# Kernel optimization log

Measured on AMD Instinct MI355X. Metric: run time of the kernel, lower is better.

## Reference

```python
import jax, jax.numpy as jnp
import numpy as np

N_PE = 100000   # num 'pe' nodes
N_R = 100000    # num 'router' nodes
E = 600000      # edges per relation
D_IN = 64       # input feature dim per node type
H = 128         # hidden_channels
G = 64          # graphs in batch


def setup_inputs() -> dict:
    key = jax.random.key(0)
    ks = jax.random.split(key, 20)
    inp = {}
    inp["x_pe"] = jax.random.normal(ks[0], (N_PE, D_IN), jnp.float32)
    inp["x_r"] = jax.random.normal(ks[1], (N_R, D_IN), jnp.float32)
    # edge_index per relation: row0 = src node ids, row1 = dst node ids
    inp["ei_per"] = jax.random.randint(ks[2], (2, E), 0, N_PE, jnp.int32)   # pe -> router
    inp["ei_rpe"] = jax.random.randint(ks[3], (2, E), 0, N_R, jnp.int32)    # router -> pe
    inp["ei_rr"] = jax.random.randint(ks[4], (2, E), 0, N_R, jnp.int32)     # router -> router
    inp["batch_pe"] = jnp.sort(jax.random.randint(ks[5], (N_PE,), 0, G, jnp.int32))
    inp["batch_r"] = jnp.sort(jax.random.randint(ks[6], (N_R,), 0, G, jnp.int32))
    # GraphConv params, relation axis ordered [pe->router, router->pe, router->router]
    s1 = 1.0 / np.sqrt(D_IN)
    s2 = 1.0 / np.sqrt(H)
    inp["Wrel1"] = jax.random.normal(ks[7], (3, D_IN, H), jnp.float32) * s1
    inp["brel1"] = jnp.zeros((3, H), jnp.float32)
    inp["Wroot1"] = jax.random.normal(ks[8], (3, D_IN, H), jnp.float32) * s1
    inp["Wrel23"] = jax.random.normal(ks[9], (2, 3, H, H), jnp.float32) * s2
    inp["brel23"] = jnp.zeros((2, 3, H), jnp.float32)
    inp["Wroot23"] = jax.random.normal(ks[10], (2, 3, H, H), jnp.float32) * s2
    # per-node-type MLP heads, type axis ordered [pe, router]
    inp["mlp_W1"] = jax.random.normal(ks[11], (2, H, 5), jnp.float32) * s2
    inp["mlp_b1"] = jnp.zeros((2, 5), jnp.float32)
    inp["mlp_W2"] = jax.random.normal(ks[12], (2, 5, 1), jnp.float32) * (1.0 / np.sqrt(5.0))
    inp["mlp_b2"] = jnp.zeros((2, 1), jnp.float32)
    inp["out_W"] = jax.random.normal(ks[13], (2, 1), jnp.float32) * (1.0 / np.sqrt(2.0))
    inp["out_b"] = jnp.zeros((1,), jnp.float32)
    return inp


def _hetero_graphconv(x_pe, x_r, ei_per, ei_rpe, ei_rr, Wrel, brel, Wroot):
    # GraphConv: lin_rel(scatter_add(x_src)) + lin_root(x_dst); to_hetero sums per dst type.
    agg_r_from_pe = jax.ops.segment_sum(x_pe[ei_per[0]], ei_per[1], num_segments=N_R)
    agg_pe_from_r = jax.ops.segment_sum(x_r[ei_rpe[0]], ei_rpe[1], num_segments=N_PE)
    agg_r_from_r = jax.ops.segment_sum(x_r[ei_rr[0]], ei_rr[1], num_segments=N_R)
    o_pe = agg_pe_from_r @ Wrel[1] + brel[1] + x_pe @ Wroot[1]
    o_r = (agg_r_from_pe @ Wrel[0] + brel[0] + x_r @ Wroot[0]) \
        + (agg_r_from_r @ Wrel[2] + brel[2] + x_r @ Wroot[2])
    return o_pe, o_r


def reference(x_pe, x_r, ei_per, ei_rpe, ei_rr, batch_pe, batch_r,
              Wrel1, brel1, Wroot1, Wrel23, brel23, Wroot23,
              mlp_W1, mlp_b1, mlp_W2, mlp_b2, out_W, out_b):
    h_pe, h_r = _hetero_graphconv(x_pe, x_r, ei_per, ei_rpe, ei_rr, Wrel1, brel1, Wroot1)
    h_pe, h_r = jax.nn.relu(h_pe), jax.nn.relu(h_r)
    h_pe, h_r = _hetero_graphconv(h_pe, h_r, ei_per, ei_rpe, ei_rr, Wrel23[0], brel23[0], Wroot23[0])
    h_pe, h_r = jax.nn.relu(h_pe), jax.nn.relu(h_r)
    h_pe, h_r = _hetero_graphconv(h_pe, h_r, ei_per, ei_rpe, ei_rr, Wrel23[1], brel23[1], Wroot23[1])
    gm_pe = jax.ops.segment_max(h_pe, batch_pe, num_segments=G)  # [G, H]
    gm_r = jax.ops.segment_max(h_r, batch_r, num_segments=G)
    def mlp(x, W1, b1, W2, b2):
        return jax.nn.relu(x @ W1 + b1) @ W2 + b2
    o_pe = mlp(gm_pe, mlp_W1[0], mlp_b1[0], mlp_W2[0], mlp_b2[0])  # [G, 1]
    o_r = mlp(gm_r, mlp_W1[1], mlp_b1[1], mlp_W2[1], mlp_b2[1])
    cat = jnp.concatenate([o_pe, o_r], axis=1)  # [G, 2]
    return cat @ out_W + out_b  # [G, 1]
```

## Files before the change

### kernel.cpp

```cpp
#include <hip/hip_runtime.h>
#include <cstddef>
#include <cstdint>

#define DIN 64
#define HID 128
#define NBKMAX 256
#define EPB 2048

typedef _Float16 half4v __attribute__((ext_vector_type(4)));
typedef _Float16 half8v __attribute__((ext_vector_type(8)));
typedef float f32x16 __attribute__((ext_vector_type(16)));

__device__ __forceinline__ unsigned encf(float f) {
    unsigned b = __float_as_uint(f);
    return (b & 0x80000000u) ? ~b : (b | 0x80000000u);
}
__device__ __forceinline__ float decf(unsigned u) {
    unsigned b = (u & 0x80000000u) ? (u & 0x7FFFFFFFu) : ~u;
    return __uint_as_float(b);
}

__global__ void conv_x2_k(const float* s0, _Float16* d0, int n40,
                          const float* s1, _Float16* d1, int n41) {
    int r = blockIdx.y;
    const float* s = r == 0 ? s0 : s1;
    _Float16* d = r == 0 ? d0 : d1;
    int n4 = r == 0 ? n40 : n41;
    int i = blockIdx.x * 256 + threadIdx.x;
    if (i >= n4) return;
    float4 v = *reinterpret_cast<const float4*>(&s[i * 4]);
    half4v h;
    h.x = (_Float16)v.x; h.y = (_Float16)v.y; h.z = (_Float16)v.z; h.w = (_Float16)v.w;
    *reinterpret_cast<half4v*>(&d[i * 4]) = h;
}

struct CW { const float* src; const float* src2; _Float16* dst; int K; int total; };
__global__ __launch_bounds__(256) void prep_k(
    CW c0, CW c1, CW c2, CW c3, CW c4, CW c5, CW c6, CW c7,
    const int* e0, const int* e1, const int* e2, int E,
    int* hc0, int* hc1, int* hc2,
    const int* bpe, int npe, int* spe,
    const int* brr, int nrr, int* srr, int G) {
    int y = blockIdx.y;
    if (y < 8) {
        CW J;
        switch (y) {
            case 0: J = c0; break; case 1: J = c1; break; case 2: J = c2; break;
            case 3: J = c3; break; case 4: J = c4; break; case 5: J = c5; break;
            case 6: J = c6; break; default: J = c7; break;
        }
        int i = blockIdx.x * 256 + threadIdx.x;
        if (i >= J.total) return;
        int m = i / (J.K * HID);
        int rem = i % (J.K * HID);
        int k = rem / HID;
        int col = rem % HID;
        float v = J.src[i];
        if (J.src2) v += J.src2[i];
        J.dst[(size_t)m * HID * J.K + (size_t)col * J.K + k] = (_Float16)v;
    } else if (y < 11) {
        int r = y - 8;
        const int* ei = r == 0 ? e0 : (r == 1 ? e1 : e2);
        int* cnt = r == 0 ? hc0 : (r == 1 ? hc1 : hc2);
        __shared__ int sc[NBKMAX];
        int t = threadIdx.x;
        sc[t] = 0;
        __syncthreads();
        int base = blockIdx.x * EPB;
        if (base >= E) return;
        int n = min(EPB, E - base);
        for (int i = t; i < n; i += 256)
            atomicAdd(&sc[(unsigned)ei[E + base + i] >> 9], 1);
        __syncthreads();
        if (sc[t]) atomicAdd(&cnt[t], sc[t]);
    } else {
        int r = blockIdx.x;
        if (r >= 2) return;
        const int* batch = r == 0 ? bpe : brr;
        int n = r == 0 ? npe : nrr;
        int* starts = r == 0 ? spe : srr;
        int g = threadIdx.x;
        if (g > G) return;
        int lo = 0, hi = n;
        while (lo < hi) {
            int mid = (lo + hi) >> 1;
            if (batch[mid] < g) lo = mid + 1; else hi = mid;
        }
        starts[g] = lo;
    }
}

__global__ __launch_bounds__(256) void bscan_k(int* c0, int* bb0, int* cu0, int* rp0, int n0,
                                               int* c1, int* bb1, int* cu1, int* rp1, int n1,
                                               int* c2, int* bb2, int* cu2, int* rp2, int n2,
                                               int E) {
    __shared__ int sh[256];
    int t = threadIdx.x;
    for (int r = 0; r < 3; ++r) {
        int* cnt = r == 0 ? c0 : (r == 1 ? c1 : c2);
        int* bb  = r == 0 ? bb0 : (r == 1 ? bb1 : bb2);
        int* cu  = r == 0 ? cu0 : (r == 1 ? cu1 : cu2);
        int* rp  = r == 0 ? rp0 : (r == 1 ? rp1 : rp2);
        int N    = r == 0 ? n0 : (r == 1 ? n1 : n2);
        int v = cnt[t];
        sh[t] = v;
        __syncthreads();
        for (int off = 1; off < 256; off <<= 1) {
            int val = (t >= off) ? sh[t - off] : 0;
            __syncthreads();
            sh[t] += val;
            __syncthreads();
        }
        int ex = sh[t] - v;
        bb[t] = ex;
        cu[t] = ex;
        if (t == 255) bb[256] = sh[255];
        if (t == 0) rp[N] = E;
        __syncthreads();
    }
}

__global__ __launch_bounds__(256) void bin_k(const int* e0, const int* e1, const int* e2, int E,
                                             int* cu0, int* cu1, int* cu2,
                                             unsigned* t0, unsigned* t1, unsigned* t2) {
    int r = blockIdx.y;
    const int* ei = r == 0 ? e0 : (r == 1 ? e1 : e2);
    int* gcur = r == 0 ? cu0 : (r == 1 ? cu1 : cu2);
    unsigned* temp = r == 0 ? t0 : (r == 1 ? t1 : t2);
    __shared__ unsigned pk[EPB];
    __shared__ unsigned short bkb[EPB];
    __shared__ int cnt[NBKMAX];
    __shared__ int scn[NBKMAX];
    __shared__ int rb[NBKMAX];
    int t = threadIdx.x;
    int base = blockIdx.x * EPB;
    int n = min(EPB, E - base);
    cnt[t] = 0;
    __syncthreads();
    for (int i = t; i < n; i += 256)
        atomicAdd(&cnt[(unsigned)ei[E + base + i] >> 9], 1);
    __syncthreads();
    {
        int v = cnt[t];
        scn[t] = v;
        __syncthreads();
        for (int off = 1; off < 256; off <<= 1) {
            int val = (t >= off) ? scn[t - off] : 0;
            __syncthreads();
            scn[t] += val;
            __syncthreads();
        }
        int ex = scn[t] - v;
        __syncthreads();
        scn[t] = ex;
    }
    {
        int c = cnt[t];
        rb[t] = c ? atomicAdd(&gcur[t], c) : 0;
        cnt[t] = 0;
    }
    __syncthreads();
    for (int i = t; i < n; i += 256) {
        int s = ei[base + i];
        int d = ei[E + base + i];
        int b = (unsigned)d >> 9;
        int slot = scn[b] + atomicAdd(&cnt[b], 1);
        pk[slot] = ((unsigned)s << 9) | (unsigned)(d & 511);
        bkb[slot] = (unsigned short)b;
    }
    __syncthreads();
    for (int i = t; i < n; i += 256) {
        int b = bkb[i];
        temp[rb[b] + (i - scn[b])] = pk[i];
    }
}

__global__ __launch_bounds__(256) void bcsr_k(const unsigned* t0, const unsigned* t1, const unsigned* t2,
                                              const int* bb0, const int* bb1, const int* bb2,
                                              int* rp0, int* rp1, int* rp2,
                                              int* a0, int* a1, int* a2,
                                              int n0, int n1, int n2) {
    int r = blockIdx.y;
    const unsigned* temp = r == 0 ? t0 : (r == 1 ? t1 : t2);
    const int* bb = r == 0 ? bb0 : (r == 1 ? bb1 : bb2);
    int* rp = r == 0 ? rp0 : (r == 1 ? rp1 : rp2);
    int* adj = r == 0 ? a0 : (r == 1 ? a1 : a2);
    int N = r == 0 ? n0 : (r == 1 ? n1 : n2);
    int b = blockIdx.x;
    int lo = bb[b], hi = bb[b + 1];
    __shared__ int cnt[512];
    __shared__ int sh[256];
    int t = threadIdx.x;
    cnt[t] = 0; cnt[t + 256] = 0;
    __syncthreads();
    for (int i = lo + t; i < hi; i += 256)
        atomicAdd(&cnt[temp[i] & 511], 1);
    __syncthreads();
    int c0 = cnt[2 * t], c1 = cnt[2 * t + 1];
    sh[t] = c0 + c1;
    __syncthreads();
    for (int off = 1; off < 256; off <<= 1) {
        int v = (t >= off) ? sh[t - off] : 0;
        __syncthreads();
        sh[t] += v;
        __syncthreads();
    }
    int pairExcl = sh[t] - (c0 + c1);
    __syncthreads();
    int e0x = lo + pairExcl;
    int e1x = e0x + c0;
    cnt[2 * t] = e0x;
    cnt[2 * t + 1] = e1x;
    int nodeBase = b * 512;
    if (nodeBase + 2 * t < N) rp[nodeBase + 2 * t] = e0x;
    if (nodeBase + 2 * t + 1 < N) rp[nodeBase + 2 * t + 1] = e1x;
    __syncthreads();
    for (int i = lo + t; i < hi; i += 256) {
        unsigned p = temp[i];
        int pos = atomicAdd(&cnt[p & 511], 1);
        adj[pos] = p >> 9;
    }
}

struct AJob { const _Float16* X; const int* rp; const int* adj; _Float16* AGG; int N; int gb; };
template <int D>
__global__ __launch_bounds__(256) void gather3_k(AJob a0, AJob a1, AJob a2) {
    int b = blockIdx.x;
    AJob J;
    if (b < a0.gb) { J = a0; }
    else if (b < a0.gb + a1.gb) { J = a1; b -= a0.gb; }
    else { J = a2; b -= a0.gb + a1.gb; }
    constexpr int TPN = D / 8;
    constexpr int NPB = 256 / TPN;
    int node = b * NPB + threadIdx.x / TPN;
    int glane = threadIdx.x % TPN;
    if (node >= J.N) return;
    int a = J.rp[node], e1 = J.rp[node + 1];
    float acc[8] = {0.f, 0.f, 0.f, 0.f, 0.f, 0.f, 0.f, 0.f};
    for (int base = a; base < e1; base += TPN) {
        int idx = base + glane;
        int myAdj = (idx < e1) ? J.adj[idx] : 0;
        int cnt = min(TPN, e1 - base);
        int j = 0;
        for (; j + 4 <= cnt; j += 4) {
            int s0 = __shfl(myAdj, j, TPN);
            int s1 = __shfl(myAdj, j + 1, TPN);
            int s2 = __shfl(myAdj, j + 2, TPN);
            int s3 = __shfl(myAdj, j + 3, TPN);
            half8v v0 = *reinterpret_cast<const half8v*>(&J.X[(size_t)s0 * D + glane * 8]);
            half8v v1 = *reinterpret_cast<const half8v*>(&J.X[(size_t)s1 * D + glane * 8]);
            half8v v2 = *reinterpret_cast<const half8v*>(&J.X[(size_t)s2 * D + glane * 8]);
            half8v v3 = *reinterpret_cast<const half8v*>(&J.X[(size_t)s3 * D + glane * 8]);
#pragma unroll
            for (int i = 0; i < 8; ++i)
                acc[i] += (float)v0[i] + (float)v1[i] + (float)v2[i] + (float)v3[i];
        }
        for (; j < cnt; ++j) {
            int s0 = __shfl(myAdj, j, TPN);
            half8v v0 = *reinterpret_cast<const half8v*>(&J.X[(size_t)s0 * D + glane * 8]);
#pragma unroll
            for (int i = 0; i < 8; ++i) acc[i] += (float)v0[i];
        }
    }
    half8v o;
#pragma unroll
    for (int i = 0; i < 8; ++i) o[i] = (_Float16)acc[i];
    *reinterpret_cast<half8v*>(&J.AGG[(size_t)node * D + glane * 8]) = o;
}

struct GJob {
    const _Float16* A0; const _Float16* A1; const _Float16* A2;
    const _Float16* W0; const _Float16* W1; const _Float16* W2;
    const float* b0; const float* b1;
    _Float16* O;
    int N; int total; int gb;
};

template <bool RELU>
__global__ __launch_bounds__(256) void gemm2_k(GJob j0, GJob j1, int K, int lg) {
    const bool second = ((int)blockIdx.x >= j0.gb);
    const GJob J = second ? j1 : j0;
    const int bx = blockIdx.x - (second ? j0.gb : 0);
    __shared__ _Float16 Alds[2][128 * 64];
    __shared__ _Float16 Wlds[2][128 * 64];
    const int tid = threadIdx.x;
    const int lane = tid & 63;
    const int w = tid >> 6;
    const int wr = w & 1, wc = w >> 1;
    const int rowBase = bx * 128;

    f32x16 acc[2][2];
#pragma unroll
    for (int r = 0; r < 2; ++r)
#pragma unroll
        for (int c = 0; c < 2; ++c)
#pragma unroll
            for (int q = 0; q < 16; ++q) acc[r][c][q] = 0.0f;

    const _Float16* Ap[3] = {J.A0, J.A1, J.A2};
    const _Float16* Wp[3] = {J.W0, J.W1, J.W2};

    int srow[4];
    int soff[4];
    int ldsoff[4];
#pragma unroll
    for (int i = 0; i < 4; ++i) {
        int r_ = (w * 4 + i) * 8 + (lane >> 3);
        srow[i] = r_;
        soff[i] = ((lane & 7) ^ (r_ & 7)) << 4;
        ldsoff[i] = (w * 4 + i) << 10;
    }

    const int total = J.total;
    const int cmask = (1 << lg) - 1;

    auto stage = [&](int c, int buf) {
        const int s = c >> lg;
        const int k0b = (c & cmask) << 7;
        const char* Ab = (const char*)Ap[s];
        const char* Wb = (const char*)Wp[s];
        char* al = (char*)&Alds[buf][0];
        char* wl = (char*)&Wlds[buf][0];
#pragma unroll
        for (int i = 0; i < 4; ++i) {
            const char* ga = Ab + ((size_t)(rowBase + srow[i]) * K) * 2 + k0b + soff[i];
            const char* gw = Wb + ((size_t)srow[i] * K) * 2 + k0b + soff[i];
            __builtin_amdgcn_global_load_lds(
                (const __attribute__((address_space(1))) void*)ga,
                (__attribute__((address_space(3))) void*)(al + ldsoff[i]), 16, 0, 0);
            __builtin_amdgcn_global_load_lds(
                (const __attribute__((address_space(1))) void*)gw,
                (__attribute__((address_space(3))) void*)(wl + ldsoff[i]), 16, 0, 0);
        }
    };

    stage(0, 0);
    asm volatile("s_waitcnt vmcnt(0)\n\ts_barrier" ::: "memory");

    const int rA0 = wr * 64 + (lane & 31);
    const int cW0 = wc * 64 + (lane & 31);
    const int ghi = lane >> 5;

    for (int c = 0; c < total; ++c) {
        if (c + 1 < total) stage(c + 1, (c + 1) & 1);
        const _Float16* al = &Alds[c & 1][0];
        const _Float16* wl = &Wlds[c & 1][0];
#pragma unroll
        for (int t = 0; t < 4; ++t) {
            const int g = 2 * t + ghi;
            half8v av[2], wv[2];
#pragma unroll
            for (int r = 0; r < 2; ++r) {
                const int row = rA0 + r * 32;
                av[r] = *reinterpret_cast<const half8v*>(al + ((row * 8 + (g ^ (row & 7))) << 3));
            }
#pragma unroll
            for (int cc = 0; cc < 2; ++cc) {
                const int col = cW0 + cc * 32;
                wv[cc] = *reinterpret_cast<const half8v*>(wl + ((col * 8 + (g ^ (col & 7))) << 3));
            }
#pragma unroll
            for (int r = 0; r < 2; ++r)
#pragma unroll
                for (int cc = 0; cc < 2; ++cc)
                    acc[r][cc] = __builtin_amdgcn_mfma_f32_32x32x16_f16(wv[cc], av[r], acc[r][cc], 0, 0, 0);
        }
        asm volatile("s_waitcnt vmcnt(0)\n\ts_barrier" ::: "memory");
    }

    const int half_ = lane >> 5;
#pragma unroll
    for (int r = 0; r < 2; ++r) {
        int node = rowBase + (wr * 2 + r) * 32 + (lane & 31);
        bool ok = (node < J.N);
        _Float16* orow = J.O + (size_t)node * HID;
#pragma unroll
        for (int cc = 0; cc < 2; ++cc) {
            int fbase = wc * 64 + cc * 32;
#pragma unroll
            for (int g = 0; g < 4; ++g) {
                int fmine = fbase + g * 8 + 4 * half_;
                float4 bv = *reinterpret_cast<const float4*>(&J.b0[fmine]);
                if (J.b1) {
                    float4 b2v = *reinterpret_cast<const float4*>(&J.b1[fmine]);
                    bv.x += b2v.x; bv.y += b2v.y; bv.z += b2v.z; bv.w += b2v.w;
                }
                union { half4v h; int i[2]; } m, p;
#pragma unroll
                for (int i = 0; i < 4; ++i) {
                    float v = acc[r][cc][g * 4 + i] + ((const float*)&bv)[i];
                    if (RELU) v = fmaxf(v, 0.f);
                    m.h[i] = (_Float16)v;
                }
                p.i[0] = __shfl_xor(m.i[0], 32);
                p.i[1] = __shfl_xor(m.i[1], 32);
                half4v lo = half_ ? p.h : m.h;
                half4v hi = half_ ? m.h : p.h;
                half8v outv;
#pragma unroll
                for (int i = 0; i < 4; ++i) { outv[i] = lo[i]; outv[4 + i] = hi[i]; }
                if (ok && ((g & 1) == half_))
                    *reinterpret_cast<half8v*>(&orow[fbase + g * 8]) = outv;
            }
        }
    }
}

__global__ __launch_bounds__(128) void seg_max2_k(const _Float16* H0, const int* st0, unsigned* g0,
                                                  const _Float16* H1, const int* st1, unsigned* g1) {
    int z = blockIdx.z;
    const _Float16* Hf = z == 0 ? H0 : H1;
    const int* starts = z == 0 ? st0 : st1;
    unsigned* gmU = z == 0 ? g0 : g1;
    int g = blockIdx.x;
    int sub = blockIdx.y;
    int SUB = gridDim.y;
    int f = threadIdx.x;
    int s0 = starts[g], s1 = starts[g + 1];
    int len = s1 - s0;
    if (len <= 0) return;
    int chunk = (len + SUB - 1) / SUB;
    int a = s0 + sub * chunk;
    int b = min(a + chunk, s1);
    if (a >= b) return;
    float m = -__builtin_huge_valf();
    for (int n = a; n < b; ++n) m = fmaxf(m, (float)Hf[(size_t)n * HID + f]);
    atomicMax(&gmU[g * HID + f], encf(m));
}

__global__ void head_k(const unsigned* __restrict__ gmU_pe, const unsigned* __restrict__ gmU_r,
                       const float* __restrict__ W1, const float* __restrict__ b1,
                       const float* __restrict__ W2, const float* __restrict__ b2,
                       const float* __restrict__ oW, const float* __restrict__ ob,
                       float* __restrict__ out, int G) {
    int g = threadIdx.x;
    if (g >= G) return;
    float vals[2];
#pragma unroll
    for (int t = 0; t < 2; ++t) {
        const unsigned* gm = t ? gmU_r : gmU_pe;
        float z[5];
#pragma unroll
        for (int j = 0; j < 5; ++j) z[j] = b1[t * 5 + j];
        for (int f = 0; f < HID; ++f) {
            float x = decf(gm[g * HID + f]);
#pragma unroll
            for (int j = 0; j < 5; ++j) z[j] = fmaf(x, W1[t * HID * 5 + f * 5 + j], z[j]);
        }
        float o = b2[t];
#pragma unroll
        for (int j = 0; j < 5; ++j) o = fmaf(fmaxf(z[j], 0.f), W2[t * 5 + j], o);
        vals[t] = o;
    }
    out[g] = vals[0] * oW[0] + vals[1] * oW[1] + ob[0];
}

extern "C" void kernel_launch(void* const* d_in, const int* in_sizes, int n_in,
                              void* d_out, int out_size, void* d_ws, size_t ws_size,
                              hipStream_t stream) {
    const float* x_pe    = (const float*)d_in[0];
    const float* x_r     = (const float*)d_in[1];
    const int* ei_per    = (const int*)d_in[2];
    const int* ei_rpe    = (const int*)d_in[3];
    const int* ei_rr     = (const int*)d_in[4];
    const int* batch_pe  = (const int*)d_in[5];
    const int* batch_r   = (const int*)d_in[6];
    const float* Wrel1   = (const float*)d_in[7];
    const float* brel1   = (const float*)d_in[8];
    const float* Wroot1  = (const float*)d_in[9];
    const float* Wrel23  = (const float*)d_in[10];
    const float* brel23  = (const float*)d_in[11];
    const float* Wroot23 = (const float*)d_in[12];
    const float* mlp_W1  = (const float*)d_in[13];
    const float* mlp_b1  = (const float*)d_in[14];
    const float* mlp_W2  = (const float*)d_in[15];
    const float* mlp_b2  = (const float*)d_in[16];
    const float* out_W   = (const float*)d_in[17];
    const float* out_b   = (const float*)d_in[18];
    float* out = (float*)d_out;

    const int N_PE = in_sizes[0] / DIN;
    const int N_R  = in_sizes[1] / DIN;
    const int E    = in_sizes[2] / 2;
    const int G    = out_size;
    const int NMAX = (N_PE > N_R) ? N_PE : N_R;
    const size_t SZM = (size_t)NMAX * HID;

    _Float16* H1 = (_Float16*)d_ws;
    _Float16* H2 = H1 + SZM;
    _Float16* H3 = H2 + SZM;
    _Float16* H4 = H3 + SZM;
    _Float16* H5 = H4 + SZM;
    _Float16* xh_pe = H5 + SZM;
    _Float16* xh_r  = xh_pe + (size_t)N_PE * DIN;
    _Float16* wt_rel1    = xh_r + (size_t)N_R * DIN;
    _Float16* wt_root1pe = wt_rel1 + 3 * DIN * HID;
    _Float16* wt_wsum1   = wt_root1pe + DIN * HID;
    _Float16* wt_rel23   = wt_wsum1 + DIN * HID;
    _Float16* wt_root_l2 = wt_rel23 + 6 * HID * HID;
    _Float16* wt_root_l3 = wt_root_l2 + HID * HID;
    _Float16* wt_wsum2   = wt_root_l3 + HID * HID;
    _Float16* wt_wsum3   = wt_wsum2 + HID * HID;
    unsigned* gmU_pe = (unsigned*)(wt_wsum3 + HID * HID);
    unsigned* gmU_r  = gmU_pe + G * HID;
    int* bktCnt = (int*)(gmU_r + G * HID);
    int* starts_pe = bktCnt + 3 * NBKMAX;
    int* starts_r  = starts_pe + (G + 1);
    int* bb     = starts_r + (G + 1);
    int* gcur   = bb + 3 * (NBKMAX + 1);
    int* csr    = gcur + 3 * NBKMAX;
    const size_t relstride = (size_t)(NMAX + 1) + 2 * (size_t)E + 16;

    int* rp[3]; int* adjp[3]; unsigned* tmp[3];
    const int Nds[3] = {N_R, N_PE, N_R};
    for (int r = 0; r < 3; ++r) {
        int* rowptr = csr + (size_t)r * relstride;
        rp[r] = rowptr;
        adjp[r] = rowptr + (Nds[r] + 1);
        tmp[r] = (unsigned*)(adjp[r] + E);
    }

    const int gpe = (N_PE + 127) / 128, grr = (N_R + 127) / 128;
    const int eb = (E + EPB - 1) / EPB;

    hipMemsetAsync(gmU_pe, 0, (2 * (size_t)G * HID + 3 * NBKMAX) * sizeof(int), stream);
    {
        int n40 = N_PE * DIN / 4, n41 = N_R * DIN / 4;
        int nmax = n40 > n41 ? n40 : n41;
        dim3 g((nmax + 255) / 256, 2);
        conv_x2_k<<<g, 256, 0, stream>>>(x_pe, xh_pe, n40, x_r, xh_r, n41);
    }
    {
        CW c0{Wrel1, nullptr, wt_rel1, DIN, 3 * DIN * HID};
        CW c1{Wroot1 + 1 * DIN * HID, nullptr, wt_root1pe, DIN, DIN * HID};
        CW c2{Wroot1, Wroot1 + 2 * DIN * HID, wt_wsum1, DIN, DIN * HID};
        CW c3{Wrel23, nullptr, wt_rel23, HID, 6 * HID * HID};
        CW c4{Wroot23 + 1 * HID * HID, nullptr, wt_root_l2, HID, HID * HID};
        CW c5{Wroot23 + 4 * HID * HID, nullptr, wt_root_l3, HID, HID * HID};
        CW c6{Wroot23, Wroot23 + 2 * HID * HID, wt_wsum2, HID, HID * HID};
        CW c7{Wroot23 + 3 * HID * HID, Wroot23 + 5 * HID * HID, wt_wsum3, HID, HID * HID};
        int gx = (6 * HID * HID + 255) / 256;
        if (eb > gx) gx = eb;
        dim3 g(gx, 12);
        prep_k<<<g, 256, 0, stream>>>(c0, c1, c2, c3, c4, c5, c6, c7,
                                      ei_per, ei_rpe, ei_rr, E,
                                      bktCnt, bktCnt + NBKMAX, bktCnt + 2 * NBKMAX,
                                      batch_pe, N_PE, starts_pe,
                                      batch_r, N_R, starts_r, G);
    }
    {
        bscan_k<<<1, 256, 0, stream>>>(
            bktCnt, bb, gcur, rp[0], Nds[0],
            bktCnt + NBKMAX, bb + (NBKMAX + 1), gcur + NBKMAX, rp[1], Nds[1],
            bktCnt + 2 * NBKMAX, bb + 2 * (NBKMAX + 1), gcur + 2 * NBKMAX, rp[2], Nds[2], E);
        dim3 gh(eb, 3);
        bin_k<<<gh, 256, 0, stream>>>(ei_per, ei_rpe, ei_rr, E,
                                      gcur, gcur + NBKMAX, gcur + 2 * NBKMAX,
                                      tmp[0], tmp[1], tmp[2]);
        dim3 gc(NBKMAX, 3);
        bcsr_k<<<gc, 256, 0, stream>>>(tmp[0], tmp[1], tmp[2],
                                       bb, bb + (NBKMAX + 1), bb + 2 * (NBKMAX + 1),
                                       rp[0], rp[1], rp[2],
                                       adjp[0], adjp[1], adjp[2],
                                       Nds[0], Nds[1], Nds[2]);
    }

    {
        AJob a0{xh_r, rp[1], adjp[1], H1, N_PE, (N_PE + 31) / 32};
        AJob a1{xh_pe, rp[0], adjp[0], H2, N_R, (N_R + 31) / 32};
        AJob a2{xh_r, rp[2], adjp[2], H3, N_R, (N_R + 31) / 32};
        gather3_k<DIN><<<a0.gb + a1.gb + a2.gb, 256, 0, stream>>>(a0, a1, a2);
        GJob jp{H1, xh_pe, nullptr,
                wt_rel1 + 1 * DIN * HID, wt_root1pe, nullptr,
                brel1 + HID, nullptr, H4, N_PE, 2, gpe};
        GJob jr{H2, H3, xh_r,
                wt_rel1, wt_rel1 + 2 * DIN * HID, wt_wsum1,
                brel1, brel1 + 2 * HID, H5, N_R, 3, grr};
        gemm2_k<true><<<gpe + grr, 256, 0, stream>>>(jp, jr, DIN, 0);
    }
    {
        AJob a0{H5, rp[1], adjp[1], H1, N_PE, (N_PE + 15) / 16};
        AJob a1{H4, rp[0], adjp[0], H2, N_R, (N_R + 15) / 16};
        AJob a2{H5, rp[2], adjp[2], H3, N_R, (N_R + 15) / 16};
        gather3_k<HID><<<a0.gb + a1.gb + a2.gb, 256, 0, stream>>>(a0, a1, a2);
        GJob jp{H1, H4, nullptr,
                wt_rel23 + 1 * HID * HID, wt_root_l2, nullptr,
                brel23 + HID, nullptr, H1, N_PE, 2 * 2, gpe};
        GJob jr{H2, H3, H5,
                wt_rel23, wt_rel23 + 2 * HID * HID, wt_wsum2,
                brel23, brel23 + 2 * HID, H2, N_R, 3 * 2, grr};
        gemm2_k<true><<<gpe + grr, 256, 0, stream>>>(jp, jr, HID, 1);
    }
    {
        AJob a0{H2, rp[1], adjp[1], H3, N_PE, (N_PE + 15) / 16};
        AJob a1{H1, rp[0], adjp[0], H4, N_R, (N_R + 15) / 16};
        AJob a2{H2, rp[2], adjp[2], H5, N_R, (N_R + 15) / 16};
        gather3_k<HID><<<a0.gb + a1.gb + a2.gb, 256, 0, stream>>>(a0, a1, a2);
        GJob jp{H3, H1, nullptr,
                wt_rel23 + 4 * HID * HID, wt_root_l3, nullptr,
                brel23 + 4 * HID, nullptr, H3, N_PE, 2 * 2, gpe};
        GJob jr{H4, H5, H2,
                wt_rel23 + 3 * HID * HID, wt_rel23 + 5 * HID * HID, wt_wsum3,
                brel23 + 3 * HID, brel23 + 5 * HID, H4, N_R, 3 * 2, grr};
        gemm2_k<false><<<gpe + grr, 256, 0, stream>>>(jp, jr, HID, 1);
    }

    dim3 gs(G, 16, 2);
    seg_max2_k<<<gs, 128, 0, stream>>>(H3, starts_pe, gmU_pe, H4, starts_r, gmU_r);
    head_k<<<1, 64, 0, stream>>>(gmU_pe, gmU_r, mlp_W1, mlp_b1, mlp_W2, mlp_b2, out_W, out_b, out, G);
}
```

Before: 547.9 us.

## Fuse per-graph segment max into final layer GEMM epilogue

```diff
diff --git a/kernel.cpp b/kernel.cpp
--- a/kernel.cpp
+++ b/kernel.cpp
@@ -274,9 +274,11 @@
     const float* b0; const float* b1;
     _Float16* O;
     int N; int total; int gb;
+    const int* batch;
+    unsigned* gmU;
 };
 
-template <bool RELU>
+template <bool RELU, bool SEGMAX>
 __global__ __launch_bounds__(256) void gemm2_k(GJob j0, GJob j1, int K, int lg) {
     const bool second = ((int)blockIdx.x >= j0.gb);
     const GJob J = second ? j1 : j0;
@@ -369,9 +371,72 @@
     }
 
     const int half_ = lane >> 5;
+    const int lane31 = lane & 31;
+
+    if constexpr (SEGMAX) {
+        const float NEGINF = -__builtin_huge_valf();
+        const int node0 = rowBase + (wr * 2) * 32 + lane31;
+        const int node1 = node0 + 32;
+        const bool ok0 = (node0 < J.N);
+        const bool ok1 = (node1 < J.N);
+        const int lastn = min(rowBase + 127, J.N - 1);
+        const int gfirst = J.batch[rowBase];
+        const int glast = J.batch[lastn];
+        if (gfirst == glast) {
+            unsigned* gbase = J.gmU + (size_t)gfirst * HID;
+#pragma unroll
+            for (int cc = 0; cc < 2; ++cc)
+#pragma unroll
+            for (int g = 0; g < 4; ++g) {
+                const int f = wc * 64 + cc * 32 + g * 8 + 4 * half_;
+                float4 bv = *reinterpret_cast<const float4*>(&J.b0[f]);
+                if (J.b1) {
+                    float4 b2v = *reinterpret_cast<const float4*>(&J.b1[f]);
+                    bv.x += b2v.x; bv.y += b2v.y; bv.z += b2v.z; bv.w += b2v.w;
+                }
+#pragma unroll
+                for (int i = 0; i < 4; ++i) {
+                    float bb_ = ((const float*)&bv)[i];
+                    float v0 = ok0 ? (acc[0][cc][g * 4 + i] + bb_) : NEGINF;
+                    float v1 = ok1 ? (acc[1][cc][g * 4 + i] + bb_) : NEGINF;
+                    float vm = fmaxf(v0, v1);
+#pragma unroll
+                    for (int off = 1; off < 32; off <<= 1)
+                        vm = fmaxf(vm, __shfl_xor(vm, off, 32));
+                    if (lane31 == 0) atomicMax(&gbase[f + i], encf(vm));
+                }
+            }
+        } else {
+#pragma unroll
+            for (int r = 0; r < 2; ++r) {
+                const int node = rowBase + (wr * 2 + r) * 32 + lane31;
+                if (node >= J.N) continue;
+                const int gid = J.batch[node];
+                unsigned* gbase = J.gmU + (size_t)gid * HID;
+#pragma unroll
+                for (int cc = 0; cc < 2; ++cc)
+#pragma unroll
+                for (int g = 0; g < 4; ++g) {
+                    const int f = wc * 64 + cc * 32 + g * 8 + 4 * half_;
+                    float4 bv = *reinterpret_cast<const float4*>(&J.b0[f]);
+                    if (J.b1) {
+                        float4 b2v = *reinterpret_cast<const float4*>(&J.b1[f]);
+                        bv.x += b2v.x; bv.y += b2v.y; bv.z += b2v.z; bv.w += b2v.w;
+                    }
+#pragma unroll
+                    for (int i = 0; i < 4; ++i) {
+                        float v = acc[r][cc][g * 4 + i] + ((const float*)&bv)[i];
+                        atomicMax(&gbase[f + i], encf(v));
+                    }
+                }
+            }
+        }
+        return;
+    }
+
 #pragma unroll
     for (int r = 0; r < 2; ++r) {
-        int node = rowBase + (wr * 2 + r) * 32 + (lane & 31);
+        int node = rowBase + (wr * 2 + r) * 32 + lane31;
         bool ok = (node < J.N);
         _Float16* orow = J.O + (size_t)node * HID;
 #pragma unroll
@@ -404,28 +469,6 @@
             }
         }
     }
-}
-
-__global__ __launch_bounds__(128) void seg_max2_k(const _Float16* H0, const int* st0, unsigned* g0,
-                                                  const _Float16* H1, const int* st1, unsigned* g1) {
-    int z = blockIdx.z;
-    const _Float16* Hf = z == 0 ? H0 : H1;
-    const int* starts = z == 0 ? st0 : st1;
-    unsigned* gmU = z == 0 ? g0 : g1;
-    int g = blockIdx.x;
-    int sub = blockIdx.y;
-    int SUB = gridDim.y;
-    int f = threadIdx.x;
-    int s0 = starts[g], s1 = starts[g + 1];
-    int len = s1 - s0;
-    if (len <= 0) return;
-    int chunk = (len + SUB - 1) / SUB;
-    int a = s0 + sub * chunk;
-    int b = min(a + chunk, s1);
-    if (a >= b) return;
-    float m = -__builtin_huge_valf();
-    for (int n = a; n < b; ++n) m = fmaxf(m, (float)Hf[(size_t)n * HID + f]);
-    atomicMax(&gmU[g * HID + f], encf(m));
 }
 
 __global__ void head_k(const unsigned* __restrict__ gmU_pe, const unsigned* __restrict__ gmU_r,
@@ -572,11 +615,11 @@
         gather3_k<DIN><<<a0.gb + a1.gb + a2.gb, 256, 0, stream>>>(a0, a1, a2);
         GJob jp{H1, xh_pe, nullptr,
                 wt_rel1 + 1 * DIN * HID, wt_root1pe, nullptr,
-                brel1 + HID, nullptr, H4, N_PE, 2, gpe};
+                brel1 + HID, nullptr, H4, N_PE, 2, gpe, nullptr, nullptr};
         GJob jr{H2, H3, xh_r,
                 wt_rel1, wt_rel1 + 2 * DIN * HID, wt_wsum1,
-                brel1, brel1 + 2 * HID, H5, N_R, 3, grr};
-        gemm2_k<true><<<gpe + grr, 256, 0, stream>>>(jp, jr, DIN, 0);
+                brel1, brel1 + 2 * HID, H5, N_R, 3, grr, nullptr, nullptr};
+        gemm2_k<true, false><<<gpe + grr, 256, 0, stream>>>(jp, jr, DIN, 0);
     }
     {
         AJob a0{H5, rp[1], adjp[1], H1, N_PE, (N_PE + 15) / 16};
@@ -585,11 +628,11 @@
         gather3_k<HID><<<a0.gb + a1.gb + a2.gb, 256, 0, stream>>>(a0, a1, a2);
         GJob jp{H1, H4, nullptr,
                 wt_rel23 + 1 * HID * HID, wt_root_l2, nullptr,
-                brel23 + HID, nullptr, H1, N_PE, 2 * 2, gpe};
+                brel23 + HID, nullptr, H1, N_PE, 2 * 2, gpe, nullptr, nullptr};
         GJob jr{H2, H3, H5,
                 wt_rel23, wt_rel23 + 2 * HID * HID, wt_wsum2,
-                brel23, brel23 + 2 * HID, H2, N_R, 3 * 2, grr};
-        gemm2_k<true><<<gpe + grr, 256, 0, stream>>>(jp, jr, HID, 1);
+                brel23, brel23 + 2 * HID, H2, N_R, 3 * 2, grr, nullptr, nullptr};
+        gemm2_k<true, false><<<gpe + grr, 256, 0, stream>>>(jp, jr, HID, 1);
     }
     {
         AJob a0{H2, rp[1], adjp[1], H3, N_PE, (N_PE + 15) / 16};
@@ -598,14 +641,12 @@
         gather3_k<HID><<<a0.gb + a1.gb + a2.gb, 256, 0, stream>>>(a0, a1, a2);
         GJob jp{H3, H1, nullptr,
                 wt_rel23 + 4 * HID * HID, wt_root_l3, nullptr,
-                brel23 + 4 * HID, nullptr, H3, N_PE, 2 * 2, gpe};
+                brel23 + 4 * HID, nullptr, nullptr, N_PE, 2 * 2, gpe, batch_pe, gmU_pe};
         GJob jr{H4, H5, H2,
                 wt_rel23 + 3 * HID * HID, wt_rel23 + 5 * HID * HID, wt_wsum3,
-                brel23 + 3 * HID, brel23 + 5 * HID, H4, N_R, 3 * 2, grr};
-        gemm2_k<false><<<gpe + grr, 256, 0, stream>>>(jp, jr, HID, 1);
-    }
-
-    dim3 gs(G, 16, 2);
-    seg_max2_k<<<gs, 128, 0, stream>>>(H3, starts_pe, gmU_pe, H4, starts_r, gmU_r);
+                brel23 + 3 * HID, brel23 + 5 * HID, nullptr, N_R, 3 * 2, grr, batch_r, gmU_r};
+        gemm2_k<false, true><<<gpe + grr, 256, 0, stream>>>(jp, jr, HID, 1);
+    }
+
     head_k<<<1, 64, 0, stream>>>(gmU_pe, gmU_r, mlp_W1, mlp_b1, mlp_W2, mlp_b2, out_W, out_b, out, G);
 }
```

Result: slower. 824.6 us (+50.5%).
